# Kernel tuning notes

Hardware: AMD Instinct MI355X
Metric: run time of the kernel (lower is better)

## Reference

```python
import jax, jax.numpy as jnp
import numpy as np

N_EMBD = 500
BLOCK_SIZE = 256


def _rope(q, k, theta=0.0001):
    # Faithful to the torch code: freq exponent uses the FULL dim C, and the
    # tensor is split into contiguous halves (not interleaved pairs).
    B, T, C = q.shape
    half = C // 2
    i = jnp.arange(half)
    freqs = theta ** (2.0 * (i // 2).astype(q.dtype) / C)  # [half]
    ang = jnp.arange(T, dtype=q.dtype)[:, None] * freqs[None, :]  # [T, half]
    cos_p, sin_p = jnp.cos(ang), jnp.sin(ang)
    q1, q2 = q[..., :half], q[..., half:]
    k1, k2 = k[..., :half], k[..., half:]
    q_rot = jnp.concatenate([q1 * cos_p - q2 * sin_p, q1 * sin_p + q2 * cos_p], axis=-1)
    k_rot = jnp.concatenate([k1 * cos_p - k2 * sin_p, k1 * sin_p + k2 * cos_p], axis=-1)
    return q_rot, k_rot


def setup_inputs() -> dict:
    key = jax.random.key(0)
    k1, k2, k3, k4 = jax.random.split(key, 4)
    B, T = 256, 256
    scale = 1.0 / np.sqrt(N_EMBD)
    x = jax.random.normal(k1, (B, T, N_EMBD), dtype=jnp.float32)
    Wq = jax.random.normal(k2, (N_EMBD, 500), dtype=jnp.float32) * scale
    Wk = jax.random.normal(k3, (N_EMBD, 500), dtype=jnp.float32) * scale
    Wv = jax.random.normal(k4, (N_EMBD, 500), dtype=jnp.float32) * scale
    return {"x": x, "Wq": Wq, "Wk": Wk, "Wv": Wv}


def reference(x, Wq, Wk, Wv):
    B, T, C = x.shape  # C == n_embd == 500
    q = jnp.einsum("btc,ch->bth", x, Wq)
    k = jnp.einsum("btc,ch->bth", x, Wk)
    q, k = _rope(q, k)
    # NOTE: original scales by input-dim C**-0.5 (500), not head_size**-0.5.
    wei = jnp.einsum("bth,bsh->bts", q, k) * (C ** -0.5)
    causal = jnp.tril(jnp.ones((T, T), dtype=bool))
    wei = jnp.where(causal, wei, -jnp.inf)
    wei = jax.nn.softmax(wei, axis=-1)
    # dropout: eval mode (identity) for deterministic reference
    v = jnp.einsum("btc,ch->bth", x, Wv)
    return jnp.einsum("bts,bsh->bth", wei, v)
```

## Files before the change

### kernel.cpp

```cpp
#include <hip/hip_runtime.h>

typedef unsigned short u16;
typedef __attribute__((ext_vector_type(8))) __bf16 bf16x8;
typedef __attribute__((ext_vector_type(4))) float f32x4;

__device__ __forceinline__ float bf2f(u16 u) {
  union { unsigned int i; float f; } v; v.i = ((unsigned int)u) << 16; return v.f;
}
__device__ __forceinline__ u16 f2bf(float f) {
  union { float f; unsigned int i; } v; v.f = f;
  unsigned int u = v.i;
  return (u16)((u + 0x7fffu + ((u >> 16) & 1u)) >> 16);
}
__device__ __forceinline__ void async16(void* lds, const void* g) {
  __builtin_amdgcn_global_load_lds(
      (const __attribute__((address_space(1))) unsigned int*)g,
      (__attribute__((address_space(3))) unsigned int*)lds, 16, 0, 0);
}

__global__ void k_convert_x(const float* __restrict__ x, u16* __restrict__ xb) {
  int idx = blockIdx.x * 256 + threadIdx.x;
  int m = idx >> 6, c0 = (idx & 63) * 8;
  u16 o[8];
  if (c0 < 496) {
    float4 v0 = *(const float4*)(x + (size_t)m * 500 + c0);
    float4 v1 = *(const float4*)(x + (size_t)m * 500 + c0 + 4);
    o[0] = f2bf(v0.x); o[1] = f2bf(v0.y); o[2] = f2bf(v0.z); o[3] = f2bf(v0.w);
    o[4] = f2bf(v1.x); o[5] = f2bf(v1.y); o[6] = f2bf(v1.z); o[7] = f2bf(v1.w);
  } else {
#pragma unroll
    for (int j = 0; j < 8; ++j) {
      int c = c0 + j;
      o[j] = f2bf((c < 500) ? x[(size_t)m * 500 + c] : 0.f);
    }
  }
  *(uint4*)(xb + (size_t)m * 512 + c0) = *(const uint4*)o;
}

__global__ void k_convert_w(const float* __restrict__ Wq, const float* __restrict__ Wk,
                            const float* __restrict__ Wv, u16* __restrict__ Wt) {
  int idx = blockIdx.x * 256 + threadIdx.x;
  int g = idx >> 18;
  int r = idx & 262143;
  int n = r >> 9, k = r & 511;
  const float* W = (g == 0) ? Wq : (g == 1) ? Wk : Wv;
  int orig = (g == 2) ? n : ((n & 1) ? (n >> 1) + 250 : (n >> 1));
  float v = (n < 500 && k < 500) ? W[(size_t)k * 500 + orig] : 0.f;
  Wt[idx] = f2bf(v);
}

__global__ void k_tables(float* __restrict__ cospair, float* __restrict__ sinpair) {
  int t = blockIdx.x, p = threadIdx.x;
  float c = 0.f, s = 0.f;
  if (p < 250) {
    float ex = (float)(2 * (p >> 1)) / 500.0f;
    float fr = powf(1e-4f, ex);
    float ang = (float)t * fr;
    c = cosf(ang); s = sinf(ang);
  }
  cospair[t * 256 + p] = c;
  sinpair[t * 256 + p] = s;
}

__global__ __launch_bounds__(512, 2) void k_gemm_qkv(
    const u16* __restrict__ xb, const u16* __restrict__ Wt,
    const float* __restrict__ cospair, const float* __restrict__ sinpair,
    u16* __restrict__ qb, u16* __restrict__ kb, u16* __restrict__ vT) {
  __shared__ u16 As[4][128][64];
  const int tid = threadIdx.x;
  const int lane = tid & 63;
  const int w = tid >> 6;
  const int wm = w >> 2, wn = w & 3;
  const int lrow = lane & 15, lhi = lane >> 4;
  const int sx = lrow & 7;

  int bid = blockIdx.x;
  int wk = (bid & 7) * 192 + (bid >> 3);
  int mg = wk / 12;
  int j12 = wk - mg * 12;
  int g = j12 >> 2, bni = j12 & 3;
  const int bn = bni << 7;
  const int m0 = mg << 9;

  const u16* Ab = xb + (size_t)m0 * 512;

  bf16x8 breg[8][2][2];
  {
    const u16* Bl = Wt + ((size_t)(g * 512 + bn + wn * 32) + lrow) * 512 + lhi * 8;
#pragma unroll
    for (int t = 0; t < 8; ++t)
#pragma unroll
      for (int ni = 0; ni < 2; ++ni)
#pragma unroll
        for (int kk2 = 0; kk2 < 2; ++kk2)
          breg[t][ni][kk2] =
              *(const bf16x8*)(Bl + (size_t)ni * 16 * 512 + t * 64 + kk2 * 32);
  }

#define STAGE(S) { int mt_ = (S) >> 3, t_ = (S) & 7, buf_ = (S) & 3;          \
    _Pragma("unroll")                                                         \
    for (int ld = 0; ld < 2; ++ld) {                                          \
      int gi = ld * 512 + tid;                                                \
      int r_ = gi >> 3, c_ = gi & 7;                                          \
      async16((char*)As + buf_ * 16384 + (size_t)gi * 16,                     \
              Ab + ((size_t)(mt_ * 128 + r_)) * 512 + t_ * 64 +               \
                  ((c_ ^ (r_ & 7)) * 8));                                     \
    } }

#define AFRAGS(S)                                                             \
    const u16* Asl = (const u16*)As + ((S) & 3) * 8192;                       \
    bf16x8 a[4][2];                                                           \
    _Pragma("unroll")                                                         \
    for (int mi = 0; mi < 4; ++mi)                                            \
      _Pragma("unroll")                                                       \
      for (int kk2 = 0; kk2 < 2; ++kk2)                                       \
        a[mi][kk2] = *(const bf16x8*)(Asl + (wm * 64 + mi * 16 + lrow) * 64 + \
                                      (((kk2 * 4 + lhi) ^ sx) * 8));

#define EPILOGUE(MT) {                                                        \
    int mb = m0 + (MT) * 128;                                                 \
    if (g < 2) {                                                              \
      u16* dst = (g == 0) ? qb : kb;                                          \
      _Pragma("unroll")                                                       \
      for (int mi = 0; mi < 4; ++mi)                                          \
        _Pragma("unroll")                                                     \
        for (int ni = 0; ni < 2; ++ni) {                                      \
          int n = bn + wn * 32 + ni * 16 + lrow;                              \
          int p = n >> 1;                                                     \
          _Pragma("unroll")                                                   \
          for (int jj = 0; jj < 4; ++jj) {                                    \
            int m = mb + wm * 64 + mi * 16 + lhi * 4 + jj;                    \
            float v = acc[mi][ni][jj];                                        \
            float o = __shfl_xor(v, 1, 64);                                   \
            int ti = (m & 255) * 256 + p;                                     \
            float c = cospair[ti], s = sinpair[ti];                           \
            float r = (n & 1) ? (o * s + v * c) : (v * c - o * s);            \
            dst[(size_t)m * 512 + n] = f2bf(r);                               \
          }                                                                   \
        }                                                                     \
    } else {                                                                  \
      _Pragma("unroll")                                                       \
      for (int mi = 0; mi < 4; ++mi)                                          \
        _Pragma("unroll")                                                     \
        for (int ni = 0; ni < 2; ++ni) {                                      \
          int n = bn + wn * 32 + ni * 16 + lrow;                              \
          _Pragma("unroll")                                                   \
          for (int jj = 0; jj < 4; ++jj) {                                    \
            int m = mb + wm * 64 + mi * 16 + lhi * 4 + jj;                    \
            vT[(size_t)(m >> 8) * 131072 + (size_t)n * 256 + (m & 255)] =     \
                f2bf(acc[mi][ni][jj]);                                        \
          }                                                                   \
        }                                                                     \
    } }

  STAGE(0); STAGE(1); STAGE(2);
  asm volatile("s_waitcnt vmcnt(4)" ::: "memory");
  __builtin_amdgcn_s_barrier();
  asm volatile("" ::: "memory");

  for (int mt = 0; mt < 3; ++mt) {
    f32x4 acc[4][2] = {};
#pragma unroll
    for (int t = 0; t < 8; ++t) {
      STAGE(mt * 8 + t + 3);
      AFRAGS(t);
      __builtin_amdgcn_s_setprio(1);
#pragma unroll
      for (int kk2 = 0; kk2 < 2; ++kk2)
#pragma unroll
        for (int mi = 0; mi < 4; ++mi)
#pragma unroll
          for (int ni = 0; ni < 2; ++ni)
            acc[mi][ni] = __builtin_amdgcn_mfma_f32_16x16x32_bf16(
                a[mi][kk2], breg[t][ni][kk2], acc[mi][ni], 0, 0, 0);
      __builtin_amdgcn_s_setprio(0);
      asm volatile("s_waitcnt vmcnt(4)" ::: "memory");
      __builtin_amdgcn_s_barrier();
      asm volatile("" ::: "memory");
    }
    EPILOGUE(mt);
  }
  {
    f32x4 acc[4][2] = {};
#pragma unroll
    for (int t = 0; t < 8; ++t) {
      if (t < 5) STAGE(27 + t);
      AFRAGS(t);
      __builtin_amdgcn_s_setprio(1);
#pragma unroll
      for (int kk2 = 0; kk2 < 2; ++kk2)
#pragma unroll
        for (int mi = 0; mi < 4; ++mi)
#pragma unroll
          for (int ni = 0; ni < 2; ++ni)
            acc[mi][ni] = __builtin_amdgcn_mfma_f32_16x16x32_bf16(
                a[mi][kk2], breg[t][ni][kk2], acc[mi][ni], 0, 0, 0);
      __builtin_amdgcn_s_setprio(0);
      if (t < 5)       asm volatile("s_waitcnt vmcnt(4)" ::: "memory");
      else if (t == 5) asm volatile("s_waitcnt vmcnt(2)" ::: "memory");
      else if (t == 6) asm volatile("s_waitcnt vmcnt(0)" ::: "memory");
      if (t < 7) {
        __builtin_amdgcn_s_barrier();
        asm volatile("" ::: "memory");
      }
    }
    EPILOGUE(3);
  }
#undef STAGE
#undef AFRAGS
#undef EPILOGUE
}

__global__ __launch_bounds__(256) void k_attn(
    const u16* __restrict__ qb, const u16* __restrict__ kb,
    const u16* __restrict__ vT, float* __restrict__ out) {
  __shared__ u16 smem[40960];
  u16* Ring = smem;
  u16* Ps = smem + 24576;

  const int tid = threadIdx.x;
  const int lane = tid & 63;
  const int w = tid >> 6;
  int bid = blockIdx.x;
  int wkk = (bid & 7) * 128 + (bid >> 3);
  const int b = wkk >> 2;
  const int qt = wkk & 3;
  const int t0 = qt * 64;
  const int lrow = lane & 15, lhi = lane >> 4;
  const int sx = lrow & 7;
  const int vxor = (lrow >> 1) & 3;
  const int NT = 4 * (qt + 1);
  const int NTB = 2 * (qt + 1);
  const int NV = 2 * NTB;

  const u16* qrow = qb + ((size_t)(b * 256 + t0 + w * 16 + lrow)) * 512;
  bf16x8 qf[16];
#pragma unroll
  for (int kk = 0; kk < 16; ++kk)
    qf[kk] = *(const bf16x8*)(qrow + kk * 32 + lhi * 8);

#define STAGE_K(ST) {                                                         \
    _Pragma("unroll")                                                         \
    for (int ld = 0; ld < 4; ++ld) {                                          \
      int gi = ld * 256 + tid;                                                \
      int r_ = gi >> 6, c_ = gi & 63;                                         \
      async16((char*)Ring + ((ST) % 3) * 16384 + (size_t)gi * 16,             \
              kb + ((size_t)(b * 256 + (ST) * 16 + r_)) * 512 +               \
                  ((c_ ^ (r_ & 7)) * 8));                                     \
    } }

#define STAGE_V(ST, HH) {                                                     \
    _Pragma("unroll")                                                         \
    for (int ld = 0; ld < 4; ++ld) {                                          \
      int gi = ld * 256 + tid;                                                \
      int r_ = gi >> 2, c_ = gi & 3;                                          \
      async16((char*)Ring + (((ST) * 2 + (HH)) % 3) * 16384 + (size_t)gi * 16,\
              vT + (size_t)b * 131072 + ((size_t)((HH) * 256 + r_)) * 256 +   \
                  (ST) * 32 + ((c_ ^ ((r_ >> 1) & 3)) * 8));                  \
    } }

  f32x4 sa[16] = {};
  STAGE_K(0); STAGE_K(1);
  asm volatile("s_waitcnt vmcnt(4)" ::: "memory");
  __builtin_amdgcn_s_barrier();
  asm volatile("" ::: "memory");
#pragma unroll
  for (int st = 0; st < 16; ++st) {
    if (st < NT) {
      if (st + 2 < NT) STAGE_K(st + 2);
      const u16* Ksl = Ring + (st % 3) * 8192 + lrow * 512;
      __builtin_amdgcn_s_setprio(1);
#pragma unroll
      for (int kk = 0; kk < 16; ++kk) {
        bf16x8 bf = *(const bf16x8*)(Ksl + ((kk * 4 + lhi) ^ sx) * 8);
        sa[st] = __builtin_amdgcn_mfma_f32_16x16x32_bf16(qf[kk], bf, sa[st], 0, 0, 0);
      }
      __builtin_amdgcn_s_setprio(0);
      if (st + 2 < NT)      asm volatile("s_waitcnt vmcnt(4)" ::: "memory");
      else if (st + 1 < NT) asm volatile("s_waitcnt vmcnt(0)" ::: "memory");
      if (st + 1 < NT) {
        __builtin_amdgcn_s_barrier();
        asm volatile("" ::: "memory");
      }
    }
  }

  const float scale = 0.04472135954999579f;
  float rmax[4] = {-1e30f, -1e30f, -1e30f, -1e30f};
#pragma unroll
  for (int n = 0; n < 16; ++n) {
    int s = n * 16 + lrow;
#pragma unroll
    for (int j = 0; j < 4; ++j) {
      int t = t0 + w * 16 + lhi * 4 + j;
      float v = sa[n][j] * scale;
      if (s > t) v = -1e30f;
      sa[n][j] = v;
      rmax[j] = fmaxf(rmax[j], v);
    }
  }
#pragma unroll
  for (int j = 0; j < 4; ++j)
#pragma unroll
    for (int msk = 1; msk < 16; msk <<= 1)
      rmax[j] = fmaxf(rmax[j], __shfl_xor(rmax[j], msk, 64));
  float rsum[4] = {0.f, 0.f, 0.f, 0.f};
#pragma unroll
  for (int n = 0; n < 16; ++n)
#pragma unroll
    for (int j = 0; j < 4; ++j) {
      float p = __expf(sa[n][j] - rmax[j]);
      sa[n][j] = p;
      rsum[j] += p;
    }
#pragma unroll
  for (int j = 0; j < 4; ++j)
#pragma unroll
    for (int msk = 1; msk < 16; msk <<= 1)
      rsum[j] += __shfl_xor(rsum[j], msk, 64);
  float rinv[4];
#pragma unroll
  for (int j = 0; j < 4; ++j) rinv[j] = 1.0f / rsum[j];

#pragma unroll
  for (int n = 0; n < 16; ++n)
#pragma unroll
    for (int j = 0; j < 4; ++j) {
      int s = n * 16 + lrow;
      int trow = w * 16 + lhi * 4 + j;
      int slot = (s >> 3) ^ (trow & 7);
      Ps[trow * 256 + slot * 8 + (s & 7)] = f2bf(sa[n][j] * rinv[j]);
    }

  __syncthreads();

  f32x4 o[2][16] = {};
  STAGE_V(0, 0); STAGE_V(0, 1);
  asm volatile("s_waitcnt vmcnt(4)" ::: "memory");
  __builtin_amdgcn_s_barrier();
  asm volatile("" ::: "memory");
#pragma unroll
  for (int st = 0; st < 8; ++st) {
    if (st < NTB) {
#pragma unroll
      for (int hh = 0; hh < 2; ++hh) {
        const int f = st * 2 + hh;
        if (f + 2 < NV) {
          if (hh == 0) STAGE_V(st + 1, 0) else STAGE_V(st + 1, 1);
        }
        bf16x8 pf = *(const bf16x8*)&Ps[(w * 16 + lrow) * 256 + ((st * 4 + lhi) ^ sx) * 8];
        const u16* Vsl = Ring + (f % 3) * 8192;
        __builtin_amdgcn_s_setprio(1);
#pragma unroll
        for (int ni = 0; ni < 16; ++ni) {
          bf16x8 vf = *(const bf16x8*)(Vsl + (ni * 16 + lrow) * 32 + (lhi ^ vxor) * 8);
          o[hh][ni] = __builtin_amdgcn_mfma_f32_16x16x32_bf16(pf, vf, o[hh][ni], 0, 0, 0);
        }
        __builtin_amdgcn_s_setprio(0);
        if (f + 2 < NV)      asm volatile("s_waitcnt vmcnt(4)" ::: "memory");
        else if (f + 1 < NV) asm volatile("s_waitcnt vmcnt(0)" ::: "memory");
        if (f + 1 < NV) {
          __builtin_amdgcn_s_barrier();
          asm volatile("" ::: "memory");
        }
      }
    }
  }
#undef STAGE_K
#undef STAGE_V

  const int tb = t0 + w * 16;
#pragma unroll
  for (int hh = 0; hh < 2; ++hh)
#pragma unroll
    for (int ni = 0; ni < 16; ++ni) {
      int h = hh * 256 + ni * 16 + lrow;
      if (h < 500) {
#pragma unroll
        for (int j = 0; j < 4; ++j) {
          int t = tb + lhi * 4 + j;
          out[((size_t)(b * 256 + t)) * 500 + h] = o[hh][ni][j];
        }
      }
    }
}

extern "C" void kernel_launch(void* const* d_in, const int* in_sizes, int n_in,
                              void* d_out, int out_size, void* d_ws, size_t ws_size,
                              hipStream_t stream) {
  const float* x  = (const float*)d_in[0];
  const float* Wq = (const float*)d_in[1];
  const float* Wk = (const float*)d_in[2];
  const float* Wv = (const float*)d_in[3];
  float* out = (float*)d_out;

  u16* xb = (u16*)d_ws;
  u16* qb = xb + 33554432;
  u16* kb = qb + 33554432;
  u16* vT = kb + 33554432;
  u16* Wt = vT + 33554432;
  float* cospair = (float*)(Wt + 786432);
  float* sinpair = cospair + 65536;

  k_convert_x<<<16384, 256, 0, stream>>>(x, xb);
  k_convert_w<<<3072, 256, 0, stream>>>(Wq, Wk, Wv, Wt);
  k_tables<<<256, 256, 0, stream>>>(cospair, sinpair);
  k_gemm_qkv<<<1536, 512, 0, stream>>>(xb, Wt, cospair, sinpair, qb, kb, vT);
  k_attn<<<1024, 256, 0, stream>>>(qb, kb, vT, out);
}
```

Before: 329.7 us.

## Stream W tiles through LDS with double buffering instead of register-resident B

The QKV GEMM kernel stops preloading the whole 128-column weight slice into registers (breg). It now async-loads W tiles into an LDS double buffer alongside the x tiles. The A pipeline shrinks from a 4-deep to a 2-deep ring with a full vmcnt(0) wait every step, and the separate last-tile loop is folded into the main loop. This frees many VGPRs, which may help occupancy under launch_bounds(512,2). The cost is extra global and LDS traffic for B on every k-step and less latency hiding.

New measurement: 371.2 us. +12.6%, slower.

```diff
diff --git a/kernel.cpp b/kernel.cpp
--- a/kernel.cpp
+++ b/kernel.cpp
@@ -66,7 +66,8 @@
     const u16* __restrict__ xb, const u16* __restrict__ Wt,
     const float* __restrict__ cospair, const float* __restrict__ sinpair,
     u16* __restrict__ qb, u16* __restrict__ kb, u16* __restrict__ vT) {
-  __shared__ u16 As[4][128][64];
+  __shared__ u16 As[2][128][64];
+  __shared__ u16 Bs[2][128][64];
   const int tid = threadIdx.x;
   const int lane = tid & 63;
   const int w = tid >> 6;
@@ -83,39 +84,19 @@
   const int m0 = mg << 9;
 
   const u16* Ab = xb + (size_t)m0 * 512;
-
-  bf16x8 breg[8][2][2];
-  {
-    const u16* Bl = Wt + ((size_t)(g * 512 + bn + wn * 32) + lrow) * 512 + lhi * 8;
-#pragma unroll
-    for (int t = 0; t < 8; ++t)
-#pragma unroll
-      for (int ni = 0; ni < 2; ++ni)
-#pragma unroll
-        for (int kk2 = 0; kk2 < 2; ++kk2)
-          breg[t][ni][kk2] =
-              *(const bf16x8*)(Bl + (size_t)ni * 16 * 512 + t * 64 + kk2 * 32);
-  }
-
-#define STAGE(S) { int mt_ = (S) >> 3, t_ = (S) & 7, buf_ = (S) & 3;          \
+  const u16* Bb = Wt + ((size_t)(g * 512 + bn)) * 512;
+
+#define STAGE(S) { int mt_ = (S) >> 3, t_ = (S) & 7, buf_ = (S) & 1;          \
     _Pragma("unroll")                                                         \
     for (int ld = 0; ld < 2; ++ld) {                                          \
       int gi = ld * 512 + tid;                                                \
       int r_ = gi >> 3, c_ = gi & 7;                                          \
+      int so_ = t_ * 64 + ((c_ ^ (r_ & 7)) * 8);                              \
       async16((char*)As + buf_ * 16384 + (size_t)gi * 16,                     \
-              Ab + ((size_t)(mt_ * 128 + r_)) * 512 + t_ * 64 +               \
-                  ((c_ ^ (r_ & 7)) * 8));                                     \
+              Ab + ((size_t)(mt_ * 128 + r_)) * 512 + so_);                   \
+      async16((char*)Bs + buf_ * 16384 + (size_t)gi * 16,                     \
+              Bb + (size_t)r_ * 512 + so_);                                   \
     } }
-
-#define AFRAGS(S)                                                             \
-    const u16* Asl = (const u16*)As + ((S) & 3) * 8192;                       \
-    bf16x8 a[4][2];                                                           \
-    _Pragma("unroll")                                                         \
-    for (int mi = 0; mi < 4; ++mi)                                            \
-      _Pragma("unroll")                                                       \
-      for (int kk2 = 0; kk2 < 2; ++kk2)                                       \
-        a[mi][kk2] = *(const bf16x8*)(Asl + (wm * 64 + mi * 16 + lrow) * 64 + \
-                                      (((kk2 * 4 + lhi) ^ sx) * 8));
 
 #define EPILOGUE(MT) {                                                        \
     int mb = m0 + (MT) * 128;                                                 \
@@ -153,17 +134,32 @@
         }                                                                     \
     } }
 
-  STAGE(0); STAGE(1); STAGE(2);
-  asm volatile("s_waitcnt vmcnt(4)" ::: "memory");
+  STAGE(0);
+  asm volatile("s_waitcnt vmcnt(0)" ::: "memory");
   __builtin_amdgcn_s_barrier();
   asm volatile("" ::: "memory");
 
-  for (int mt = 0; mt < 3; ++mt) {
+  for (int mt = 0; mt < 4; ++mt) {
     f32x4 acc[4][2] = {};
 #pragma unroll
     for (int t = 0; t < 8; ++t) {
-      STAGE(mt * 8 + t + 3);
-      AFRAGS(t);
+      const int S = mt * 8 + t;
+      if (S + 1 < 32) STAGE(S + 1);
+      const u16* Asl = (const u16*)As + (t & 1) * 8192;
+      const u16* Bsl = (const u16*)Bs + (t & 1) * 8192;
+      bf16x8 a[4][2], bfr[2][2];
+#pragma unroll
+      for (int mi = 0; mi < 4; ++mi)
+#pragma unroll
+        for (int kk2 = 0; kk2 < 2; ++kk2)
+          a[mi][kk2] = *(const bf16x8*)(Asl + (wm * 64 + mi * 16 + lrow) * 64 +
+                                        (((kk2 * 4 + lhi) ^ sx) * 8));
+#pragma unroll
+      for (int ni = 0; ni < 2; ++ni)
+#pragma unroll
+        for (int kk2 = 0; kk2 < 2; ++kk2)
+          bfr[ni][kk2] = *(const bf16x8*)(Bsl + (wn * 32 + ni * 16 + lrow) * 64 +
+                                          (((kk2 * 4 + lhi) ^ sx) * 8));
       __builtin_amdgcn_s_setprio(1);
 #pragma unroll
       for (int kk2 = 0; kk2 < 2; ++kk2)
@@ -172,42 +168,15 @@
 #pragma unroll
           for (int ni = 0; ni < 2; ++ni)
             acc[mi][ni] = __builtin_amdgcn_mfma_f32_16x16x32_bf16(
-                a[mi][kk2], breg[t][ni][kk2], acc[mi][ni], 0, 0, 0);
+                a[mi][kk2], bfr[ni][kk2], acc[mi][ni], 0, 0, 0);
       __builtin_amdgcn_s_setprio(0);
-      asm volatile("s_waitcnt vmcnt(4)" ::: "memory");
+      asm volatile("s_waitcnt vmcnt(0)" ::: "memory");
       __builtin_amdgcn_s_barrier();
       asm volatile("" ::: "memory");
     }
     EPILOGUE(mt);
   }
-  {
-    f32x4 acc[4][2] = {};
-#pragma unroll
-    for (int t = 0; t < 8; ++t) {
-      if (t < 5) STAGE(27 + t);
-      AFRAGS(t);
-      __builtin_amdgcn_s_setprio(1);
-#pragma unroll
-      for (int kk2 = 0; kk2 < 2; ++kk2)
-#pragma unroll
-        for (int mi = 0; mi < 4; ++mi)
-#pragma unroll
-          for (int ni = 0; ni < 2; ++ni)
-            acc[mi][ni] = __builtin_amdgcn_mfma_f32_16x16x32_bf16(
-                a[mi][kk2], breg[t][ni][kk2], acc[mi][ni], 0, 0, 0);
-      __builtin_amdgcn_s_setprio(0);
-      if (t < 5)       asm volatile("s_waitcnt vmcnt(4)" ::: "memory");
-      else if (t == 5) asm volatile("s_waitcnt vmcnt(2)" ::: "memory");
-      else if (t == 6) asm volatile("s_waitcnt vmcnt(0)" ::: "memory");
-      if (t < 7) {
-        __builtin_amdgcn_s_barrier();
-        asm volatile("" ::: "memory");
-      }
-    }
-    EPILOGUE(3);
-  }
 #undef STAGE
-#undef AFRAGS
 #undef EPILOGUE
 }
 
```
